# Performance work log

Hardware: AMD Instinct MI355X
Metric: run time of the kernel (lower is better)

## Reference

```python
import jax, jax.numpy as jnp
import numpy as np

GRID_SIZE = 5
SPLINE_ORDER = 3
ALPHA = 0.2


def _make_grid(in_features, dtype=jnp.float32):
    # uniform grid on [-1, 1] extended by spline_order on each side
    h = 2.0 / GRID_SIZE
    pts = jnp.arange(-SPLINE_ORDER, GRID_SIZE + SPLINE_ORDER + 1, dtype=dtype) * h - 1.0
    return jnp.broadcast_to(pts, (in_features, pts.shape[0]))  # [in, G+2k+1]


def _b_splines(x, grid):
    # x: [N, in] -> bases: [N, in, GRID_SIZE + SPLINE_ORDER]
    x = x[..., None]  # [N, in, 1]
    bases = ((x >= grid[:, :-1]) & (x < grid[:, 1:])).astype(x.dtype)
    for k in range(1, SPLINE_ORDER + 1):
        left = (x - grid[:, : -(k + 1)]) / (grid[:, k:-1] - grid[:, : -(k + 1)])
        right = (grid[:, k + 1 :] - x) / (grid[:, k + 1 :] - grid[:, 1:-k])
        bases = left * bases[..., :-1] + right * bases[..., 1:]
    return bases


def _kan(x, base_weight, spline_weight):
    # efficient-KAN layer: silu base linear + B-spline linear
    N, Fin = x.shape
    Fout = base_weight.shape[0]
    grid = _make_grid(Fin, x.dtype)
    bases = _b_splines(x, grid)  # [N, in, C]
    base_out = jax.nn.silu(x) @ base_weight.T
    spline_out = bases.reshape(N, -1) @ spline_weight.reshape(Fout, -1).T
    return base_out + spline_out


def setup_inputs() -> dict:
    key = jax.random.key(0)
    k1, k2, k3, k4, k5, k6 = jax.random.split(key, 6)
    N, E, Fin, Fout = 50000, 800000, 128, 128
    C = GRID_SIZE + SPLINE_ORDER
    h = jax.random.normal(k1, (N, Fin), dtype=jnp.float32)
    edge_index = jax.random.randint(k2, (2, E), 0, N, dtype=jnp.int64)
    W = jax.random.normal(k3, (Fin, Fout), dtype=jnp.float32) * (1.414 / np.sqrt(Fin))
    a = jax.random.normal(k4, (2 * Fout, 1), dtype=jnp.float32) * 0.1
    base_weight = jax.random.normal(k5, (Fout, Fin), dtype=jnp.float32) / np.sqrt(Fin)
    spline_weight = jax.random.normal(k6, (Fout, Fin, C), dtype=jnp.float32) * 0.1
    return {"h": h, "edge_index": edge_index, "W": W, "a": a,
            "base_weight": base_weight, "spline_weight": spline_weight}


def reference(h, edge_index, W, a, base_weight, spline_weight):
    N = h.shape[0]
    Fout = W.shape[1]
    HW = h @ W                                # [N, Fout]
    HW_KAN = _kan(h, base_weight, spline_weight)  # [N, Fout]
    row, col = edge_index[0], edge_index[1]
    # cat([HW_i, HW_j]) @ a == HW_i @ a[:Fout] + HW_j @ a[Fout:]; precompute per node
    s_src = HW @ a[:Fout, 0]                  # [N]
    s_dst = HW @ a[Fout:, 0]                  # [N]
    e = jax.nn.leaky_relu(s_src[row] + s_dst[col], ALPHA)  # [E]
    # segment softmax grouped by row
    m = jax.ops.segment_max(e, row, num_segments=N)
    e_exp = jnp.exp(e - m[row])
    denom = jax.ops.segment_sum(e_exp, row, num_segments=N)
    att = e_exp / denom[row]                  # [E] (dropout inactive in eval)
    out = jax.ops.segment_sum(att[:, None] * HW_KAN[col], row, num_segments=N)
    return out
```

## Files before the change

### kernel.cpp

```cpp
#include <hip/hip_runtime.h>
#include <hip/hip_bf16.h>
#include <math.h>

#define NCHUNK 9
#define BM 128
#define NTHR 512
#define PREPB ((NCHUNK * 128 * 128) / 256)
#define PHA 256
#define PERBK 48
#define NBUKP 256
#define NBUKMAX 512

typedef __attribute__((ext_vector_type(4))) float f32x4;
typedef __attribute__((ext_vector_type(8))) short bf16x8;
typedef unsigned int u32;
typedef unsigned long long u64;

__device__ __forceinline__ unsigned short f2bf(float f) {
    u32 u = __builtin_bit_cast(u32, f);
    u32 r = (u + 0x7FFFu + ((u >> 16) & 1u)) >> 16;
    return (unsigned short)r;
}

__device__ __forceinline__ float siluf(float x) {
    return x / (1.0f + __expf(-x));
}

__global__ void k_prep(const float* __restrict__ bw, const float* __restrict__ sw,
                       const float* __restrict__ W, const float* __restrict__ a,
                       unsigned short* __restrict__ Bsw, float* __restrict__ wa,
                       const int* __restrict__ erow, const int* __restrict__ ecol,
                       int* __restrict__ counts, u32* __restrict__ binned,
                       int* __restrict__ pbcnt, int E, int nbuk, int per) {
    int bid = blockIdx.x;
    if (bid < PREPB) {
        int i = bid * 256 + threadIdx.x;
        int j = i & 7;
        int s = (i >> 3) & 15;
        int o = (i >> 7) & 127;
        int c = i >> 14;
        int k = c * 128 + (((s ^ (o & 7)) << 3) | j);
        float v = (k < 128) ? bw[o * 128 + k] : sw[o * 1024 + (k - 128)];
        Bsw[i] = f2bf(v);
        return;
    }
    if (bid == PREPB) {
        int fi = threadIdx.x;
        if (fi < 128) {
            float s1 = 0.f, s2 = 0.f;
            for (int o = 0; o < 128; ++o) {
                float w = W[fi * 128 + o];
                s1 = fmaf(w, a[o], s1);
                s2 = fmaf(w, a[128 + o], s2);
            }
            wa[fi] = s1;
            wa[128 + fi] = s2;
        }
        return;
    }
    __shared__ int cnt[NBUKMAX];
    int pb = bid - PREPB - 1;
    int e0 = pb * per;
    int e1 = min(e0 + per, E);
    for (int i = threadIdx.x; i < nbuk; i += 256) cnt[i] = 0;
    __syncthreads();
    for (int e = e0 + threadIdx.x; e < e1; e += 256) {
        int r = erow[e], c = ecol[e];
        atomicAdd(&counts[r], 1);
        int b = r >> 8;
        int pos = atomicAdd(&cnt[b], 1);
        if (pos < PERBK)
            binned[(size_t)b * (PHA * PERBK) + pb * PERBK + pos] =
                ((u32)c << 8) | (u32)(r & 255);
    }
    __syncthreads();
    for (int i = threadIdx.x; i < nbuk; i += 256)
        pbcnt[pb * NBUKP + i] = min(cnt[i], PERBK);
}

__global__ __launch_bounds__(NTHR) void k_nodes(const float* __restrict__ h,
                                                const unsigned short* __restrict__ Bsw,
                                                const float* __restrict__ wa,
                                                unsigned short* __restrict__ kanb,
                                                float* __restrict__ s_src,
                                                float* __restrict__ s_dst, int N, int nbn,
                                                const u32* __restrict__ binned,
                                                const int* __restrict__ pbcnt,
                                                int* __restrict__ cursor,
                                                int* __restrict__ colss) {
    __shared__ unsigned short A_lds[BM * 128];
    __shared__ unsigned short B_lds[128 * 128];
    __shared__ int scnt[PHA];
    const int tid = threadIdx.x;
    const int wid = tid >> 6, lane = tid & 63;

    if (blockIdx.x >= nbn) {
        int b = blockIdx.x - nbn;
        int rowbase = b << 8;
        for (int pb = tid; pb < PHA; pb += NTHR) scnt[pb] = pbcnt[pb * NBUKP + b];
        __syncthreads();
        const u32* src = binned + (size_t)b * (PHA * PERBK);
        for (int pb = wid; pb < PHA; pb += 8) {
            int n = scnt[pb];
            if (lane < n) {
                u32 pk = src[pb * PERBK + lane];
                int r = rowbase + (int)(pk & 255u);
                int pos = atomicAdd(&cursor[r], 1);
                colss[pos] = (int)(pk >> 8);
            }
        }
        return;
    }

    const int gm0 = blockIdx.x * BM;

    const int gm = tid >> 2, gq = tid & 3;
    const float* ghr = h + (size_t)min(gm0 + gm, N - 1) * 128;

    const int wm0 = (wid >> 1) * 32;
    const int wn0 = (wid & 1) * 64;
    f32x4 acc[2][4];
#pragma unroll
    for (int im = 0; im < 2; ++im)
#pragma unroll
        for (int in = 0; in < 4; ++in) acc[im][in] = {0.f, 0.f, 0.f, 0.f};

    f32x4 pf = {0.f, 0.f, 0.f, 0.f};
    for (int chunk = 0; chunk < NCHUNK; ++chunk) {
        {
            const char* gsrc = (const char*)Bsw + (size_t)chunk * 32768 + wid * 4096 + lane * 16;
            char* ldst = (char*)B_lds + wid * 4096;
#pragma unroll
            for (int i = 0; i < 4; ++i) {
                __builtin_amdgcn_global_load_lds(
                    (const __attribute__((address_space(1))) u32*)(gsrc + i * 1024),
                    (__attribute__((address_space(3))) u32*)(ldst + i * 1024), 16, 0, 0);
            }
        }
        f32x4 pfn = pf;
        if (chunk <= 7) pfn = *(const f32x4*)(ghr + chunk * 16 + gq * 4);

        if (chunk == 0) {
            f32x4 xv[8];
#pragma unroll
            for (int v = 0; v < 8; ++v) xv[v] = *(const f32x4*)(ghr + gq * 32 + v * 4);
            float s1 = 0.f, s2 = 0.f;
#pragma unroll
            for (int v = 0; v < 8; ++v) {
                f32x4 w1 = *(const f32x4*)(wa + gq * 32 + v * 4);
                f32x4 w2 = *(const f32x4*)(wa + 128 + gq * 32 + v * 4);
#pragma unroll
                for (int j = 0; j < 4; ++j) {
                    s1 = fmaf(xv[v][j], w1[j], s1);
                    s2 = fmaf(xv[v][j], w2[j], s2);
                }
            }
            s1 += __shfl_xor(s1, 1, 64); s1 += __shfl_xor(s1, 2, 64);
            s2 += __shfl_xor(s2, 1, 64); s2 += __shfl_xor(s2, 2, 64);
            int grow = gm0 + gm;
            if (gq == 0 && grow < N) {
                s_src[grow] = s1;
                s_dst[grow] = s2;
            }
#pragma unroll
            for (int sl = 0; sl < 4; ++sl) {
                int s = gq * 4 + sl;
                unsigned short pk[8];
#pragma unroll
                for (int j = 0; j < 4; ++j) {
                    pk[j] = f2bf(siluf(xv[2 * sl][j]));
                    pk[4 + j] = f2bf(siluf(xv[2 * sl + 1][j]));
                }
                *(bf16x8*)((char*)A_lds + gm * 256 + (((s ^ (gm & 7)) & 15) << 4)) =
                    *(bf16x8*)pk;
            }
        } else {
#pragma unroll
            for (int j = 0; j < 4; ++j) {
                float x = pf[j];
                float t = (x + 2.2f) * 2.5f;
                float fl = floorf(t);
                int i0 = (int)fl;
                float u = t - fl;
                float um = 1.0f - u;
                float u2 = u * u, u3 = u2 * u;
                const float c6 = 1.0f / 6.0f;
                float w0 = um * um * um * c6;
                float w1 = (3.f * u3 - 6.f * u2 + 4.f) * c6;
                float w2 = (-3.f * u3 + 3.f * u2 + 3.f * u + 1.f) * c6;
                float w3 = u3 * c6;
                u64 Wp = (u64)f2bf(w0) | ((u64)f2bf(w1) << 16) |
                         ((u64)f2bf(w2) << 32) | ((u64)f2bf(w3) << 48);
                int sh = (i0 - 3) * 16;
                u64 lo = 0, hi = 0;
                if (sh >= 0) {
                    if (sh < 64) {
                        lo = Wp << sh;
                        hi = sh ? (Wp >> (64 - sh)) : 0;
                    } else if (sh < 128) {
                        hi = Wp << (sh - 64);
                    }
                } else {
                    int r = -sh;
                    if (r < 64) lo = Wp >> r;
                }
                int s = gq * 4 + j;
                ulonglong2 pv; pv.x = lo; pv.y = hi;
                *(ulonglong2*)((char*)A_lds + gm * 256 + (((s ^ (gm & 7)) & 15) << 4)) = pv;
            }
        }
        __syncthreads();

#pragma unroll
        for (int kk = 0; kk < 4; ++kk) {
            bf16x8 af[2], bfr[4];
#pragma unroll
            for (int im = 0; im < 2; ++im) {
                int mrow = wm0 + im * 16 + (lane & 15);
                int slot = (kk * 4 + (lane >> 4)) ^ (mrow & 7);
                af[im] = *(const bf16x8*)((const char*)A_lds + mrow * 256 + slot * 16);
            }
#pragma unroll
            for (int in = 0; in < 4; ++in) {
                int orow = wn0 + in * 16 + (lane & 15);
                int slot = (kk * 4 + (lane >> 4)) ^ (orow & 7);
                bfr[in] = *(const bf16x8*)((const char*)B_lds + orow * 256 + slot * 16);
            }
#pragma unroll
            for (int im = 0; im < 2; ++im)
#pragma unroll
                for (int in = 0; in < 4; ++in)
                    acc[im][in] = __builtin_amdgcn_mfma_f32_16x16x32_bf16(
                        af[im], bfr[in], acc[im][in], 0, 0, 0);
        }
        __syncthreads();
        pf = pfn;
    }

#pragma unroll
    for (int im = 0; im < 2; ++im) {
        int rbase = wm0 + im * 16 + ((lane >> 4) << 2);
#pragma unroll
        for (int in = 0; in < 4; ++in) {
            int col = wn0 + in * 16 + (lane & 15);
#pragma unroll
            for (int r = 0; r < 4; ++r) {
                int row = rbase + r;
                int byte = row * 256 + ((col * 2) ^ (((row >> 2) & 3) << 5));
                *(unsigned short*)((char*)A_lds + byte) = f2bf(acc[im][in][r]);
            }
        }
    }
    __syncthreads();
    for (int i = tid; i < BM * 16; i += NTHR) {
        int row = i >> 4, s = i & 15;
        int byte = row * 256 + ((s << 4) ^ (((row >> 2) & 3) << 5));
        bf16x8 v = *(bf16x8*)((char*)A_lds + byte);
        int grow = gm0 + row;
        if (grow < N) *(bf16x8*)((char*)kanb + (size_t)grow * 256 + s * 16) = v;
    }
}

__global__ void k_scan1(const int* __restrict__ counts, int* __restrict__ bsum, int N) {
    int tid = threadIdx.x;
    int idx = blockIdx.x * 256 + tid;
    int v = (idx < N) ? counts[idx] : 0;
#pragma unroll
    for (int off = 32; off; off >>= 1) v += __shfl_xor(v, off, 64);
    __shared__ int ws[4];
    if ((tid & 63) == 0) ws[tid >> 6] = v;
    __syncthreads();
    if (tid == 0) bsum[blockIdx.x] = ws[0] + ws[1] + ws[2] + ws[3];
}

__global__ __launch_bounds__(1024) void k_scan2(const int* __restrict__ bsum,
                                                int* __restrict__ ebase,
                                                int* __restrict__ offsN, int nb) {
    __shared__ int ws[16];
    __shared__ int tot;
    int tid = threadIdx.x;
    int lane = tid & 63, w = tid >> 6;
    int v = (tid < nb) ? bsum[tid] : 0;
    int inc = v;
#pragma unroll
    for (int off = 1; off < 64; off <<= 1) {
        int t = __shfl_up(inc, off, 64);
        if (lane >= off) inc += t;
    }
    if (lane == 63) ws[w] = inc;
    __syncthreads();
    if (w == 0 && lane < 16) {
        int x = ws[lane];
#pragma unroll
        for (int off = 1; off < 16; off <<= 1) {
            int t = __shfl_up(x, off, 64);
            if (lane >= off) x += t;
        }
        ws[lane] = x;
        if (lane == 15) tot = x;
    }
    __syncthreads();
    int wb = w ? ws[w - 1] : 0;
    if (tid < nb) ebase[tid] = wb + inc - v;
    if (tid == 0) offsN[0] = tot;
}

__global__ void k_scan3(const int* __restrict__ counts, const int* __restrict__ ebase,
                        int* __restrict__ offsets, int* __restrict__ cursor, int N) {
    int tid = threadIdx.x;
    int idx = blockIdx.x * 256 + tid;
    int v = (idx < N) ? counts[idx] : 0;
    int lane = tid & 63, w = tid >> 6;
    int inc = v;
#pragma unroll
    for (int off = 1; off < 64; off <<= 1) {
        int t = __shfl_up(inc, off, 64);
        if (lane >= off) inc += t;
    }
    __shared__ int ws[4];
    if (lane == 63) ws[w] = inc;
    __syncthreads();
    int wb = 0;
    for (int i = 0; i < w; ++i) wb += ws[i];
    if (idx < N) {
        int off = ebase[blockIdx.x] + wb + inc - v;
        offsets[idx] = off;
        cursor[idx] = off;
    }
}

__global__ __launch_bounds__(256) void k_aggr(const int* __restrict__ offsets,
                                              int* __restrict__ cols,
                                              const float* __restrict__ s_src,
                                              const float* __restrict__ s_dst,
                                              const unsigned short* __restrict__ kanb,
                                              float* __restrict__ out, int N) {
    int wid = (blockIdx.x * 256 + threadIdx.x) >> 6;
    int lane = threadIdx.x & 63;
    if (wid >= N) return;
    int start = offsets[wid], end = offsets[wid + 1];
    int deg = end - start;
    float acc0 = 0.f, acc1 = 0.f;
    if (deg > 0) {
        float ssrc = s_src[wid];
        if (deg <= 64) {
            int key = 0x7fffffff;
            if (lane < deg) key = cols[start + lane];
#pragma unroll
            for (int k = 2; k <= 64; k <<= 1) {
#pragma unroll
                for (int j = k >> 1; j > 0; j >>= 1) {
                    int other = __shfl_xor(key, j, 64);
                    bool asc = ((lane & k) == 0);
                    bool lowr = ((lane & j) == 0);
                    int mn = min(key, other), mx = max(key, other);
                    key = (asc == lowr) ? mn : mx;
                }
            }
            float e = -3.402823466e38f;
            if (lane < deg) {
                e = ssrc + s_dst[key];
                e = (e >= 0.f) ? e : 0.2f * e;
            }
            float m = e;
#pragma unroll
            for (int off = 32; off; off >>= 1) m = fmaxf(m, __shfl_xor(m, off, 64));
            float ex = (lane < deg) ? __expf(e - m) : 0.f;
            float s = ex;
#pragma unroll
            for (int off = 32; off; off >>= 1) s += __shfl_xor(s, off, 64);
            float att = ex / s;
            u32 pbuf[8];
            float wbuf[8];
#pragma unroll
            for (int t = 0; t < 8; ++t) {
                int qc = (t < deg) ? t : 0;
                int c = __shfl(key, qc, 64);
                wbuf[t] = (t < deg) ? __shfl(att, qc, 64) : 0.f;
                pbuf[t] = ((const u32*)(kanb + (size_t)c * 128))[lane];
            }
            for (int q0 = 0; q0 < deg; q0 += 8) {
                u32 pc[8];
                float wc[8];
#pragma unroll
                for (int t = 0; t < 8; ++t) { pc[t] = pbuf[t]; wc[t] = wbuf[t]; }
                if (q0 + 8 < deg) {
#pragma unroll
                    for (int t = 0; t < 8; ++t) {
                        int q = q0 + 8 + t;
                        int qc = (q < deg) ? q : 0;
                        int c = __shfl(key, qc, 64);
                        wbuf[t] = (q < deg) ? __shfl(att, qc, 64) : 0.f;
                        pbuf[t] = ((const u32*)(kanb + (size_t)c * 128))[lane];
                    }
                }
#pragma unroll
                for (int t = 0; t < 8; ++t) {
                    float lo = __builtin_bit_cast(float, pc[t] << 16);
                    float hi = __builtin_bit_cast(float, pc[t] & 0xffff0000u);
                    acc0 = fmaf(wc[t], lo, acc0);
                    acc1 = fmaf(wc[t], hi, acc1);
                }
            }
        } else {
            if (lane == 0) {
                for (int i = start + 1; i < end; ++i) {
                    int v = cols[i];
                    int j = i - 1;
                    while (j >= start && cols[j] > v) { cols[j + 1] = cols[j]; --j; }
                    cols[j + 1] = v;
                }
            }
            __threadfence();
            float m = -3.402823466e38f;
            for (int j = start + lane; j < end; j += 64) {
                float e = ssrc + s_dst[cols[j]];
                e = (e >= 0.f) ? e : 0.2f * e;
                m = fmaxf(m, e);
            }
#pragma unroll
            for (int off = 32; off; off >>= 1) m = fmaxf(m, __shfl_xor(m, off, 64));
            float s = 0.f;
            for (int j = start + lane; j < end; j += 64) {
                float e = ssrc + s_dst[cols[j]];
                e = (e >= 0.f) ? e : 0.2f * e;
                s += __expf(e - m);
            }
#pragma unroll
            for (int off = 32; off; off >>= 1) s += __shfl_xor(s, off, 64);
            float inv = 1.0f / s;
            for (int t = start; t < end; t += 64) {
                int j = t + lane;
                float att = 0.f;
                int myc = 0;
                if (j < end) {
                    myc = cols[j];
                    float e = ssrc + s_dst[myc];
                    e = (e >= 0.f) ? e : 0.2f * e;
                    att = __expf(e - m) * inv;
                }
                int cnt = min(64, end - t);
                for (int q = 0; q < cnt; ++q) {
                    float w = __shfl(att, q, 64);
                    int c = __shfl(myc, q, 64);
                    u32 p = ((const u32*)(kanb + (size_t)c * 128))[lane];
                    float lo = __builtin_bit_cast(float, p << 16);
                    float hi = __builtin_bit_cast(float, p & 0xffff0000u);
                    acc0 = fmaf(w, lo, acc0);
                    acc1 = fmaf(w, hi, acc1);
                }
            }
        }
    }
    float2 o2 = make_float2(acc0, acc1);
    *(float2*)(out + (size_t)wid * 128 + lane * 2) = o2;
}

extern "C" void kernel_launch(void* const* d_in, const int* in_sizes, int n_in,
                              void* d_out, int out_size, void* d_ws, size_t ws_size,
                              hipStream_t stream) {
    const float* h  = (const float*)d_in[0];
    const int*   ei = (const int*)d_in[1];
    const float* W  = (const float*)d_in[2];
    const float* a  = (const float*)d_in[3];
    const float* bw = (const float*)d_in[4];
    const float* sw = (const float*)d_in[5];
    float* out = (float*)d_out;
    const int N = in_sizes[0] / 128;
    const int E = in_sizes[1] / 2;
    const int nb = (N + 255) / 256;
    const int nbn = (N + BM - 1) / BM;
    const int nbuk = (N + 255) >> 8;
    const int per = (E + PHA - 1) / PHA;

    char* ws = (char*)d_ws;
    auto alloc = [&](size_t bytes) {
        char* p = ws;
        ws += (bytes + 255) & ~(size_t)255;
        return p;
    };
    unsigned short* Bsw = (unsigned short*)alloc((size_t)NCHUNK * 128 * 128 * 2);
    float* wa    = (float*)alloc(256 * 4);
    float* ssrc  = (float*)alloc((size_t)N * 4);
    float* sdst  = (float*)alloc((size_t)N * 4);
    unsigned short* kanb = (unsigned short*)alloc((size_t)N * 128 * 2);
    int* counts  = (int*)alloc((size_t)N * 4);
    int* cursor  = (int*)alloc((size_t)N * 4);
    int* offsets = (int*)alloc(((size_t)N + 1) * 4);
    int* colss   = (int*)alloc((size_t)E * 4);
    u32* binned  = (u32*)alloc((size_t)nbuk * PHA * PERBK * 4);
    int* pbcnt   = (int*)alloc((size_t)PHA * NBUKP * 4);
    int* bsum    = (int*)alloc((size_t)nb * 4);
    int* ebase   = (int*)alloc((size_t)nb * 4);

    hipMemsetAsync(counts, 0, (size_t)N * 4, stream);

    k_prep<<<PREPB + 1 + PHA, 256, 0, stream>>>(bw, sw, W, a, Bsw, wa,
                                                ei, ei + E, counts, binned, pbcnt,
                                                E, nbuk, per);
    k_scan1<<<nb, 256, 0, stream>>>(counts, bsum, N);
    k_scan2<<<1, 1024, 0, stream>>>(bsum, ebase, offsets + N, nb);
    k_scan3<<<nb, 256, 0, stream>>>(counts, ebase, offsets, cursor, N);
    k_nodes<<<nbn + nbuk, NTHR, 0, stream>>>(h, Bsw, wa, kanb, ssrc, sdst, N, nbn,
                                             binned, pbcnt, cursor, colss);
    k_aggr<<<(N + 3) / 4, 256, 0, stream>>>(offsets, colss, ssrc, sdst, kanb, out, N);
}
```

Baseline: 153.7 us.

## Use LDS cursors for CSR scatter, move score dots to epilogue, nontemporal stores

The CSR fill step now keeps per-bucket row cursors in LDS, seeded from offsets, instead of doing global atomics on a separate cursor array. The cursor array and its initialization in the scan are removed, and pbcnt is transposed so each bucket reads its counts contiguously. The s_src/s_dst dot products move out of the chunk-0 prologue into the GEMM epilogue, using wave-wide shuffle reductions over rows reloaded from h. Output and colss writes use nontemporal stores. The trade-off is extra h reloads and register pressure in the node kernel.

```diff
diff --git a/kernel.cpp b/kernel.cpp
--- a/kernel.cpp
+++ b/kernel.cpp
@@ -8,7 +8,6 @@
 #define PREPB ((NCHUNK * 128 * 128) / 256)
 #define PHA 256
 #define PERBK 48
-#define NBUKP 256
 #define NBUKMAX 512
 
 typedef __attribute__((ext_vector_type(4))) float f32x4;
@@ -75,7 +74,7 @@
     }
     __syncthreads();
     for (int i = threadIdx.x; i < nbuk; i += 256)
-        pbcnt[pb * NBUKP + i] = min(cnt[i], PERBK);
+        pbcnt[(size_t)i * PHA + pb] = min(cnt[i], PERBK);
 }
 
 __global__ __launch_bounds__(NTHR) void k_nodes(const float* __restrict__ h,
@@ -86,10 +85,11 @@
                                                 float* __restrict__ s_dst, int N, int nbn,
                                                 const u32* __restrict__ binned,
                                                 const int* __restrict__ pbcnt,
-                                                int* __restrict__ cursor,
+                                                const int* __restrict__ offsets,
                                                 int* __restrict__ colss) {
     __shared__ unsigned short A_lds[BM * 128];
     __shared__ unsigned short B_lds[128 * 128];
+    __shared__ int lcur[256];
     __shared__ int scnt[PHA];
     const int tid = threadIdx.x;
     const int wid = tid >> 6, lane = tid & 63;
@@ -97,16 +97,19 @@
     if (blockIdx.x >= nbn) {
         int b = blockIdx.x - nbn;
         int rowbase = b << 8;
-        for (int pb = tid; pb < PHA; pb += NTHR) scnt[pb] = pbcnt[pb * NBUKP + b];
+        for (int i = tid; i < 256; i += NTHR) {
+            int r = rowbase + i;
+            lcur[i] = (r < N) ? offsets[r] : 0;
+        }
+        for (int pb = tid; pb < PHA; pb += NTHR) scnt[pb] = pbcnt[(size_t)b * PHA + pb];
         __syncthreads();
         const u32* src = binned + (size_t)b * (PHA * PERBK);
         for (int pb = wid; pb < PHA; pb += 8) {
             int n = scnt[pb];
             if (lane < n) {
                 u32 pk = src[pb * PERBK + lane];
-                int r = rowbase + (int)(pk & 255u);
-                int pos = atomicAdd(&cursor[r], 1);
-                colss[pos] = (int)(pk >> 8);
+                int pos = atomicAdd(&lcur[pk & 255u], 1);
+                __builtin_nontemporal_store((int)(pk >> 8), &colss[pos]);
             }
         }
         return;
@@ -144,24 +147,6 @@
             f32x4 xv[8];
 #pragma unroll
             for (int v = 0; v < 8; ++v) xv[v] = *(const f32x4*)(ghr + gq * 32 + v * 4);
-            float s1 = 0.f, s2 = 0.f;
-#pragma unroll
-            for (int v = 0; v < 8; ++v) {
-                f32x4 w1 = *(const f32x4*)(wa + gq * 32 + v * 4);
-                f32x4 w2 = *(const f32x4*)(wa + 128 + gq * 32 + v * 4);
-#pragma unroll
-                for (int j = 0; j < 4; ++j) {
-                    s1 = fmaf(xv[v][j], w1[j], s1);
-                    s2 = fmaf(xv[v][j], w2[j], s2);
-                }
-            }
-            s1 += __shfl_xor(s1, 1, 64); s1 += __shfl_xor(s1, 2, 64);
-            s2 += __shfl_xor(s2, 1, 64); s2 += __shfl_xor(s2, 2, 64);
-            int grow = gm0 + gm;
-            if (gq == 0 && grow < N) {
-                s_src[grow] = s1;
-                s_dst[grow] = s2;
-            }
 #pragma unroll
             for (int sl = 0; sl < 4; ++sl) {
                 int s = gq * 4 + sl;
@@ -237,6 +222,17 @@
         pf = pfn;
     }
 
+    float wa0 = wa[lane], wa1 = wa[64 + lane];
+    float wa2 = wa[128 + lane], wa3 = wa[192 + lane];
+    float sx0[16], sx1[16];
+    const int r0 = gm0 + wid * 16;
+#pragma unroll
+    for (int rr = 0; rr < 16; ++rr) {
+        const float* hr = h + (size_t)min(r0 + rr, N - 1) * 128;
+        sx0[rr] = hr[lane];
+        sx1[rr] = hr[64 + lane];
+    }
+
 #pragma unroll
     for (int im = 0; im < 2; ++im) {
         int rbase = wm0 + im * 16 + ((lane >> 4) << 2);
@@ -258,6 +254,22 @@
         bf16x8 v = *(bf16x8*)((char*)A_lds + byte);
         int grow = gm0 + row;
         if (grow < N) *(bf16x8*)((char*)kanb + (size_t)grow * 256 + s * 16) = v;
+    }
+
+#pragma unroll
+    for (int rr = 0; rr < 16; ++rr) {
+        float s1 = fmaf(sx0[rr], wa0, sx1[rr] * wa1);
+        float s2 = fmaf(sx0[rr], wa2, sx1[rr] * wa3);
+#pragma unroll
+        for (int off = 32; off; off >>= 1) {
+            s1 += __shfl_xor(s1, off, 64);
+            s2 += __shfl_xor(s2, off, 64);
+        }
+        int grow = r0 + rr;
+        if (lane == 0 && grow < N) {
+            s_src[grow] = s1;
+            s_dst[grow] = s2;
+        }
     }
 }
 
@@ -306,7 +318,7 @@
 }
 
 __global__ void k_scan3(const int* __restrict__ counts, const int* __restrict__ ebase,
-                        int* __restrict__ offsets, int* __restrict__ cursor, int N) {
+                        int* __restrict__ offsets, int N) {
     int tid = threadIdx.x;
     int idx = blockIdx.x * 256 + tid;
     int v = (idx < N) ? counts[idx] : 0;
@@ -322,11 +334,7 @@
     __syncthreads();
     int wb = 0;
     for (int i = 0; i < w; ++i) wb += ws[i];
-    if (idx < N) {
-        int off = ebase[blockIdx.x] + wb + inc - v;
-        offsets[idx] = off;
-        cursor[idx] = off;
-    }
+    if (idx < N) offsets[idx] = ebase[blockIdx.x] + wb + inc - v;
 }
 
 __global__ __launch_bounds__(256) void k_aggr(const int* __restrict__ offsets,
@@ -452,8 +460,8 @@
             }
         }
     }
-    float2 o2 = make_float2(acc0, acc1);
-    *(float2*)(out + (size_t)wid * 128 + lane * 2) = o2;
+    u64 pv = (u64)__builtin_bit_cast(u32, acc0) | ((u64)__builtin_bit_cast(u32, acc1) << 32);
+    __builtin_nontemporal_store(pv, (u64*)(out + (size_t)wid * 128 + lane * 2));
 }
 
 extern "C" void kernel_launch(void* const* d_in, const int* in_sizes, int n_in,
@@ -485,11 +493,10 @@
     float* sdst  = (float*)alloc((size_t)N * 4);
     unsigned short* kanb = (unsigned short*)alloc((size_t)N * 128 * 2);
     int* counts  = (int*)alloc((size_t)N * 4);
-    int* cursor  = (int*)alloc((size_t)N * 4);
     int* offsets = (int*)alloc(((size_t)N + 1) * 4);
     int* colss   = (int*)alloc((size_t)E * 4);
     u32* binned  = (u32*)alloc((size_t)nbuk * PHA * PERBK * 4);
-    int* pbcnt   = (int*)alloc((size_t)PHA * NBUKP * 4);
+    int* pbcnt   = (int*)alloc((size_t)nbuk * PHA * 4);
     int* bsum    = (int*)alloc((size_t)nb * 4);
     int* ebase   = (int*)alloc((size_t)nb * 4);
 
@@ -500,8 +507,8 @@
                                                 E, nbuk, per);
     k_scan1<<<nb, 256, 0, stream>>>(counts, bsum, N);
     k_scan2<<<1, 1024, 0, stream>>>(bsum, ebase, offsets + N, nb);
-    k_scan3<<<nb, 256, 0, stream>>>(counts, ebase, offsets, cursor, N);
+    k_scan3<<<nb, 256, 0, stream>>>(counts, ebase, offsets, N);
     k_nodes<<<nbn + nbuk, NTHR, 0, stream>>>(h, Bsw, wa, kanb, ssrc, sdst, N, nbn,
-                                             binned, pbcnt, cursor, colss);
+                                             binned, pbcnt, offsets, colss);
     k_aggr<<<(N + 3) / 4, 256, 0, stream>>>(offsets, colss, ssrc, sdst, kanb, out, N);
 }
```

Result: faster. 142.3 us, median of 2 (-7.4%).
